# Kernel optimization log

Measured on AMD Instinct MI355X. Metric: run time of the kernel, lower is better.

The kernel has to match this reference:

```python
import jax, jax.numpy as jnp
import numpy as np

HEAD_DIM = 64
N_HEADS = 16
DIM = 1024
EPS = 1e-6
GRID = 32  # make_axial_pos(32, 32)


def _make_theta(head_dim=HEAD_DIM, n_heads=N_HEADS):
    hd8 = head_dim // 8
    nh2 = n_heads // 2
    freqs = np.exp(np.linspace(np.log(np.pi), np.log(10 * np.pi), hd8 * nh2 + 1)[:-1])
    freqs = freqs.reshape(hd8, nh2).T  # (nh2, hd8)
    # axial positions on a 32x32 grid, cell centers in [-1, 1]
    p = np.linspace(-1.0, 1.0, GRID + 1)
    p = (p[:-1] + p[1:]) / 2
    pos = np.stack(np.meshgrid(p, p, indexing='ij'), axis=-1).reshape(GRID * GRID, 2)
    pos = np.concatenate([np.zeros((1, 2)), pos], axis=0)  # (1025, 2)
    th1 = np.concatenate([pos[:-1, None, 0:1] * freqs, pos[:-1, None, 1:2] * freqs], axis=-1)
    th2 = np.concatenate([pos[1:, None, 0:1] * freqs, pos[1:, None, 1:2] * freqs], axis=-1)
    # (seq=1024, n_heads, head_dim//4)
    return np.concatenate([th1, th2], axis=1).astype(np.float32)


def setup_inputs() -> dict:
    key = jax.random.key(0)
    k1, k2, k3 = jax.random.split(key, 3)
    B, S = 8, 1024
    x = jax.random.normal(k1, (B, S, DIM), dtype=jnp.float32)
    scale = jnp.ones((DIM,), dtype=jnp.float32)
    w_qkv = jax.random.normal(k2, (3 * DIM, DIM), dtype=jnp.float32) * 0.02
    w_out = jax.random.normal(k3, (DIM, DIM), dtype=jnp.float32) * 0.02
    theta = jnp.asarray(_make_theta())
    return {"x": x, "scale": scale, "w_qkv": w_qkv, "w_out": w_out, "theta": theta}


def _rms_norm(x, scale, eps):
    xf = x.astype(jnp.float32)
    mean_sq = jnp.mean(xf * xf, axis=-1, keepdims=True)
    s = scale.astype(jnp.float32) * jax.lax.rsqrt(mean_sq + eps)
    return x * s.astype(x.dtype)


def _rope(x, theta):
    # x: (B, H, S, D); theta: (H, S, d) with d = D // 4 -> rotates first D//2 dims
    d = theta.shape[-1]
    cos = jnp.cos(theta)
    sin = jnp.sin(theta)
    x1, x2, rest = x[..., :d], x[..., d:2 * d], x[..., 2 * d:]
    y1 = x1 * cos - x2 * sin
    y2 = x2 * cos + x1 * sin
    return jnp.concatenate([y1, y2, rest], axis=-1)


def reference(x, scale, w_qkv, w_out, theta):
    B, S, dim = x.shape
    H = N_HEADS
    D = dim // H
    skip = x
    xn = _rms_norm(x, scale, EPS)
    qkv = xn @ w_qkv.T                                  # (B, S, 3*dim)
    qkv = qkv.reshape(B, S, 3, H, D).transpose(0, 3, 2, 1, 4)  # (B, H, 3, S, D)
    q, k, v = qkv[:, :, 0], qkv[:, :, 1], qkv[:, :, 2]  # (B, H, S, D)
    th = theta[:S].transpose(1, 0, 2)                   # (H, S, D//4)
    q = _rope(q, th)
    k = _rope(k, th)
    scores = jnp.einsum('bhsd,bhtd->bhst', q, k) / jnp.sqrt(jnp.float32(D))
    causal = jnp.tril(jnp.ones((S, S), dtype=bool))
    scores = jnp.where(causal, scores, jnp.finfo(scores.dtype).min)
    attn = jax.nn.softmax(scores, axis=-1)
    o = jnp.einsum('bhst,bhtd->bhsd', attn, v)          # (B, H, S, D)
    o = o.transpose(0, 2, 1, 3).reshape(B, S, dim)
    return o @ w_out.T + skip
```

## Files before the change

kernel.cpp:

```cpp
#include <hip/hip_runtime.h>
#include <hip/hip_bf16.h>
#include <cstdint>

typedef short short8 __attribute__((ext_vector_type(8)));
typedef float f32x4 __attribute__((ext_vector_type(4)));
typedef unsigned uint4v __attribute__((ext_vector_type(4)));

#define MFMA16(a, b, c) __builtin_amdgcn_mfma_f32_16x16x32_bf16((a), (b), (c), 0, 0, 0)

__device__ __forceinline__ unsigned short f2b(float f) {
    __hip_bfloat16 h = __float2bfloat16(f);
    return __builtin_bit_cast(unsigned short, h);
}

__device__ __forceinline__ void gl_lds16(const void* g, void* l) {
    __builtin_amdgcn_global_load_lds((const __attribute__((address_space(1))) void*)g,
                                     (__attribute__((address_space(3))) void*)l, 16, 0, 0);
}

#define QSC 0.18033688011112042f

__global__ void rmsnorm_kernel(const float* __restrict__ x, const float* __restrict__ scale,
                               unsigned short* __restrict__ xn) {
    const int row = blockIdx.x;
    const int tid = threadIdx.x;
    const float4* xr = (const float4*)(x + (size_t)row * 1024);
    float4 vx = xr[tid];
    float ss = vx.x * vx.x + vx.y * vx.y + vx.z * vx.z + vx.w * vx.w;
#pragma unroll
    for (int m = 1; m < 64; m <<= 1) ss += __shfl_xor(ss, m);
    __shared__ float wsum[4];
    if ((tid & 63) == 0) wsum[tid >> 6] = ss;
    __syncthreads();
    float tot = wsum[0] + wsum[1] + wsum[2] + wsum[3];
    float rs = rsqrtf(tot * (1.0f / 1024.0f) + 1e-6f);
    const float4* sr = (const float4*)scale;
    float4 sv = sr[tid];
    ushort4 r;
    r.x = f2b(vx.x * sv.x * rs);
    r.y = f2b(vx.y * sv.y * rs);
    r.z = f2b(vx.z * sv.z * rs);
    r.w = f2b(vx.w * sv.w * rs);
    *(ushort4*)(xn + (size_t)row * 1024 + tid * 4) = r;
}

__global__ void f2b_kernel(const float* __restrict__ in, unsigned short* __restrict__ outp, int n4) {
    int i = blockIdx.x * 256 + threadIdx.x;
    if (i < n4) {
        float4 vv = ((const float4*)in)[i];
        ushort4 r;
        r.x = f2b(vv.x);
        r.y = f2b(vv.y);
        r.z = f2b(vv.z);
        r.w = f2b(vv.w);
        ((ushort4*)outp)[i] = r;
    }
}

constexpr int BM = 128, BN = 128, BK = 64, KDIM = 1024, NT = KDIM / BK;

template <int EPI>
__launch_bounds__(256, 4) __global__
    void gemm_bt(const unsigned short* __restrict__ A, const unsigned short* __restrict__ Bw,
                 unsigned short* __restrict__ qo, unsigned short* __restrict__ ko,
                 unsigned short* __restrict__ vo, const float* __restrict__ skip,
                 float* __restrict__ out, const float* __restrict__ theta) {
    __shared__ unsigned short As[BM * BK];
    __shared__ unsigned short Bs[BN * BK];
    const int tid = threadIdx.x;
    const int lane = tid & 63, w = tid >> 6;
    const int wr = w >> 1, wc = w & 1;
    const int lr = lane & 15, lg = lane >> 4;
    constexpr int NBX = (EPI == 0) ? 24 : 8;
    const int f = blockIdx.x;
    const int xcd = f & 7, wloc = f >> 3;
    const int g = xcd * (NBX * 8) + wloc;
    const int bx = g % NBX, by = g / NBX;
    const int m0 = by * BM;
    const int n0 = bx * BN;
    const int NCOL = (EPI == 0) ? 3072 : 1024;

    f32x4 acc[4][4] = {};

    auto stage = [&](int kt) {
        const int k0 = kt * BK;
#pragma unroll
        for (int i = 0; i < 4; ++i) {
            int seg = i * 256 + tid;
            int row = seg >> 3, c8 = (seg & 7) ^ (row & 7);
            gl_lds16(A + (size_t)(m0 + row) * KDIM + k0 + c8 * 8, &As[(i * 256 + w * 64) * 8]);
            gl_lds16(Bw + (size_t)(n0 + row) * KDIM + k0 + c8 * 8, &Bs[(i * 256 + w * 64) * 8]);
        }
    };

    for (int kt = 0; kt < NT; ++kt) {
        stage(kt);
        __syncthreads();
#pragma unroll
        for (int kkc = 0; kkc < 2; ++kkc) {
            short8 a[4], b[4];
            const int slot = ((kkc * 4 + lg) ^ (lr & 7)) * 8;
#pragma unroll
            for (int m = 0; m < 4; ++m)
                a[m] = *(const short8*)&As[(wr * 64 + m * 16 + lr) * BK + slot];
#pragma unroll
            for (int n = 0; n < 4; ++n)
                b[n] = *(const short8*)&Bs[(wc * 64 + n * 16 + lr) * BK + slot];
#pragma unroll
            for (int m = 0; m < 4; ++m)
#pragma unroll
                for (int n = 0; n < 4; ++n) acc[m][n] = MFMA16(a[m], b[n], acc[m][n]);
        }
        __syncthreads();
    }

    if (EPI == 0) {
        const int colb = n0 + wc * 64;
        const int c = colb >> 10, h = (colb >> 6) & 15;
#pragma unroll
        for (int m = 0; m < 4; ++m) {
            int grow0 = m0 + wr * 64 + m * 16 + lg * 4;
            int b = grow0 >> 10, s0 = grow0 & 1023;
            if (c == 2) {
#pragma unroll
                for (int n = 0; n < 4; ++n) {
                    int d = n * 16 + lr;
                    ushort4 r;
                    r.x = f2b(acc[m][n][0]);
                    r.y = f2b(acc[m][n][1]);
                    r.z = f2b(acc[m][n][2]);
                    r.w = f2b(acc[m][n][3]);
                    *(ushort4*)&vo[(((size_t)(b * 16 + h)) * 64 + d) * 1024 + s0] = r;
                }
            } else {
                unsigned short* dst = (c == 0) ? qo : ko;
                float sc = (c == 0) ? QSC : 1.0f;
#pragma unroll
                for (int j = 0; j < 4; ++j) {
                    int s = s0 + j;
                    float th = theta[((s * 16 + h) << 4) + lr];
                    float sn, cs;
                    __sincosf(th, &sn, &cs);
                    float x1 = acc[m][0][j], x2 = acc[m][1][j];
                    size_t rowb = (((size_t)(b * 16 + h)) * 1024 + s) * 64;
                    dst[rowb + lr]      = f2b((x1 * cs - x2 * sn) * sc);
                    dst[rowb + 16 + lr] = f2b((x2 * cs + x1 * sn) * sc);
                    dst[rowb + 32 + lr] = f2b(acc[m][2][j] * sc);
                    dst[rowb + 48 + lr] = f2b(acc[m][3][j] * sc);
                }
            }
        }
    } else {
#pragma unroll
        for (int m = 0; m < 4; ++m)
#pragma unroll
            for (int n = 0; n < 4; ++n) {
                int gcol = n0 + wc * 64 + n * 16 + lr;
#pragma unroll
                for (int j = 0; j < 4; ++j) {
                    int grow = m0 + wr * 64 + m * 16 + lg * 4 + j;
                    size_t idx = (size_t)grow * NCOL + gcol;
                    out[idx] = acc[m][n][j] + skip[idx];
                }
            }
    }
}

__launch_bounds__(512, 4) __global__
    void attn_kernel(const unsigned short* __restrict__ q, const unsigned short* __restrict__ k,
                     const unsigned short* __restrict__ vt, unsigned short* __restrict__ o) {
    constexpr int S = 1024, D = 64;
    __shared__ unsigned short Ks[2][64 * 64];
    __shared__ unsigned short Vs[2][64 * 64];
    __shared__ float Lls[8][32];
    const int tid = threadIdx.x, lane = tid & 63, w = tid >> 6;
    const int lr = lane & 15, lg = lane >> 4;
    const int f = blockIdx.x;
    constexpr int qmap4[4] = {3, 2, 0, 1};
    const int qb = qmap4[f >> 7];
    const int bh = (f & 7) * 16 + ((f >> 3) & 15);
    const int qs = qb * 256;
    const size_t base = (size_t)bh * (S * D);
    const int wrow0 = qs + w * 32;

    short8 qf[2][2];
#pragma unroll
    for (int m = 0; m < 2; ++m) {
        const unsigned short* qp = q + base + (size_t)(wrow0 + m * 16 + lr) * D;
        qf[m][0] = *(const short8*)(qp + lg * 8);
        qf[m][1] = *(const short8*)(qp + 32 + lg * 8);
    }

    f32x4 of[2][4] = {};
    float mrun[2] = {-1e30f, -1e30f};
    float lrun[2] = {0.f, 0.f};

    const int nkt = 4 * qb + 4;

    const int srow = tid >> 3, sc8 = (tid & 7) ^ (srow & 7);
    auto stageK = [&](int buf, int kt) {
        gl_lds16(k + base + (size_t)(kt * 64 + srow) * D + sc8 * 8, &Ks[buf][w * 512]);
    };
    auto stageV = [&](int buf, int kt) {
        gl_lds16(vt + base + (size_t)srow * S + kt * 64 + sc8 * 8, &Vs[buf][w * 512]);
    };

    stageK(0, 0);
    stageV(0, 0);
    __syncthreads();

    for (int kt = 0; kt < nkt; ++kt) {
        const int b = kt & 1;
        if (kt + 1 < nkt) {
            stageK(b ^ 1, kt + 1);
            stageV(b ^ 1, kt + 1);
        }

        if (kt * 64 <= wrow0 + 31) {
            f32x4 sf[2][4] = {};
            __builtin_amdgcn_s_setprio(1);
#pragma unroll
            for (int n = 0; n < 4; ++n) {
                const int r = n * 16 + lr;
#pragma unroll
                for (int kkc = 0; kkc < 2; ++kkc) {
                    short8 kf = *(const short8*)&Ks[b][r * 64 + (((kkc * 4 + lg) ^ (lr & 7)) * 8)];
#pragma unroll
                    for (int m = 0; m < 2; ++m) sf[m][n] = MFMA16(kf, qf[m][kkc], sf[m][n]);
                }
            }
            __builtin_amdgcn_s_setprio(0);

            if (kt * 64 + 63 > wrow0) {
#pragma unroll
                for (int m = 0; m < 2; ++m)
#pragma unroll
                    for (int n = 0; n < 4; ++n)
#pragma unroll
                        for (int j = 0; j < 4; ++j) {
                            int t = kt * 64 + 16 * n + lg * 4 + j;
                            int qr = wrow0 + m * 16 + lr;
                            if (t > qr) sf[m][n][j] = -1e30f;
                        }
            }

#pragma unroll
            for (int m = 0; m < 2; ++m) {
                float mx = -1e30f;
#pragma unroll
                for (int n = 0; n < 4; ++n)
                    mx = fmaxf(mx, fmaxf(fmaxf(sf[m][n][0], sf[m][n][1]),
                                         fmaxf(sf[m][n][2], sf[m][n][3])));
                mx = fmaxf(mx, __shfl_xor(mx, 16));
                mx = fmaxf(mx, __shfl_xor(mx, 32));

                if (__any(mx > mrun[m] + 8.0f)) {
                    float newm = fmaxf(mrun[m], mx);
                    float sc = __builtin_amdgcn_exp2f(mrun[m] - newm);
                    mrun[m] = newm;
                    float psum = 0.f;
#pragma unroll
                    for (int n = 0; n < 4; ++n)
#pragma unroll
                        for (int j = 0; j < 4; ++j) {
                            float p = __builtin_amdgcn_exp2f(sf[m][n][j] - newm);
                            sf[m][n][j] = p;
                            psum += p;
                        }
                    lrun[m] = lrun[m] * sc + psum;
#pragma unroll
                    for (int n2 = 0; n2 < 4; ++n2) of[m][n2] *= sc;
                } else {
                    float mo = mrun[m];
                    float psum = 0.f;
#pragma unroll
                    for (int n = 0; n < 4; ++n)
#pragma unroll
                        for (int j = 0; j < 4; ++j) {
                            float p = __builtin_amdgcn_exp2f(sf[m][n][j] - mo);
                            sf[m][n][j] = p;
                            psum += p;
                        }
                    lrun[m] += psum;
                }
            }

            short8 pa[2][2];
#pragma unroll
            for (int m = 0; m < 2; ++m) {
                unsigned Dk[4][2];
#pragma unroll
                for (int n = 0; n < 4; ++n)
#pragma unroll
                    for (int w2 = 0; w2 < 2; ++w2)
                        Dk[n][w2] = (unsigned)f2b(sf[m][n][2 * w2]) |
                                    ((unsigned)f2b(sf[m][n][2 * w2 + 1]) << 16);
#pragma unroll
                for (int n1 = 0; n1 < 2; ++n1) {
                    unsigned fr[4];
#pragma unroll
                    for (int w2 = 0; w2 < 2; ++w2) {
                        unsigned X0 = Dk[2 * n1][w2];
                        unsigned X1 = Dk[2 * n1 + 1][w2];
                        asm("v_permlane32_swap_b32 %0, %1" : "+v"(X0), "+v"(X1));
                        asm("v_permlane16_swap_b32 %0, %1" : "+v"(X0), "+v"(X1));
                        fr[w2] = X0;
                        fr[2 + w2] = X1;
                    }
                    uint4v t4 = {fr[0], fr[1], fr[2], fr[3]};
                    pa[m][n1] = __builtin_bit_cast(short8, t4);
                }
            }

            __builtin_amdgcn_s_setprio(1);
#pragma unroll
            for (int kkc = 0; kkc < 2; ++kkc) {
#pragma unroll
                for (int n2 = 0; n2 < 4; ++n2) {
                    const int r = n2 * 16 + lr;
                    short8 bv = *(const short8*)&Vs[b][r * 64 + (((kkc * 4 + lg) ^ (lr & 7)) * 8)];
#pragma unroll
                    for (int m = 0; m < 2; ++m) of[m][n2] = MFMA16(pa[m][kkc], bv, of[m][n2]);
                }
            }
            __builtin_amdgcn_s_setprio(0);
        }

        __syncthreads();
    }

#pragma unroll
    for (int m = 0; m < 2; ++m) {
        float l = lrun[m];
        l += __shfl_xor(l, 16);
        l += __shfl_xor(l, 32);
        Lls[w][m * 16 + lr] = l;
    }
    const int bb = bh >> 4, h = bh & 15;
#pragma unroll
    for (int m = 0; m < 2; ++m)
#pragma unroll
        for (int j = 0; j < 4; ++j) {
            float inv = 1.f / Lls[w][m * 16 + lg * 4 + j];
            int orow = wrow0 + m * 16 + lg * 4 + j;
            size_t ob = ((size_t)(bb * 1024 + orow)) * 1024 + h * 64;
#pragma unroll
            for (int n2 = 0; n2 < 4; ++n2)
                o[ob + n2 * 16 + lr] = f2b(of[m][n2][j] * inv);
        }
}

extern "C" void kernel_launch(void* const* d_in, const int* in_sizes, int n_in, void* d_out,
                              int out_size, void* d_ws, size_t ws_size, hipStream_t stream) {
    const float* x = (const float*)d_in[0];
    const float* scale = (const float*)d_in[1];
    const float* w_qkv = (const float*)d_in[2];
    const float* w_out = (const float*)d_in[3];
    const float* theta = (const float*)d_in[4];
    float* out = (float*)d_out;

    char* p = (char*)d_ws;
    unsigned short* xn = (unsigned short*)p;      p += (size_t)8192 * 1024 * 2;
    unsigned short* wqb = (unsigned short*)p;     p += (size_t)3072 * 1024 * 2;
    unsigned short* wob = (unsigned short*)p;     p += (size_t)1024 * 1024 * 2;
    unsigned short* qb_ = (unsigned short*)p;     p += (size_t)128 * 1024 * 64 * 2;
    unsigned short* kb_ = (unsigned short*)p;     p += (size_t)128 * 1024 * 64 * 2;
    unsigned short* vb_ = (unsigned short*)p;     p += (size_t)128 * 1024 * 64 * 2;
    unsigned short* ob_ = (unsigned short*)p;     p += (size_t)8192 * 1024 * 2;

    rmsnorm_kernel<<<8192, 256, 0, stream>>>(x, scale, xn);
    f2b_kernel<<<3072, 256, 0, stream>>>(w_qkv, wqb, 786432);
    f2b_kernel<<<1024, 256, 0, stream>>>(w_out, wob, 262144);
    gemm_bt<0><<<1536, 256, 0, stream>>>(xn, wqb, qb_, kb_, vb_, nullptr, nullptr, theta);
    attn_kernel<<<512, 512, 0, stream>>>(qb_, kb_, vb_, ob_);
    gemm_bt<1><<<512, 256, 0, stream>>>(ob_, wob, nullptr, nullptr, nullptr, x, out, nullptr);
}
```

Baseline: 151.8 us.

## Replace QKV GEMM with 256x256-tile 8-wave kernel and phased double buffering

```diff
diff --git a/kernel.cpp b/kernel.cpp
--- a/kernel.cpp
+++ b/kernel.cpp
@@ -166,6 +166,168 @@
     }
 }
 
+__launch_bounds__(512, 2) __global__
+    void gemm256_qkv(const unsigned short* __restrict__ A, const unsigned short* __restrict__ Bw,
+                     unsigned short* __restrict__ qo, unsigned short* __restrict__ ko,
+                     unsigned short* __restrict__ vo, const float* __restrict__ theta) {
+    __shared__ unsigned short As[2][256 * 64];
+    __shared__ unsigned short Bs[2][256 * 64];
+    const int tid = threadIdx.x;
+    const int lane = tid & 63, w = tid >> 6;
+    const int wm = w >> 2, wn = w & 3;
+    const int lr = lane & 15, lg = lane >> 4;
+    const int f = blockIdx.x;
+    const int xcd = f & 7, wloc = f >> 3;
+    const int g = xcd * 48 + wloc;
+    const int bx = g % 12, by = g / 12;
+    const int m0 = by * 256, n0 = bx * 256;
+
+    f32x4 acc[2][2][4][2] = {};
+
+#define STAGE_A(buf, kt, h)                                                            \
+    {                                                                                  \
+        _Pragma("unroll") for (int i = 0; i < 2; ++i) {                                \
+            int seg = i * 512 + tid;                                                   \
+            int row = seg >> 3, cs = (seg & 7) ^ (row & 7);                            \
+            gl_lds16(A + (size_t)(m0 + (h)*128 + row) * 1024 + (kt)*64 + cs * 8,       \
+                     &As[buf][(h)*8192 + (i * 512 + w * 64) * 8]);                     \
+        }                                                                              \
+    }
+#define STAGE_B(buf, kt, h)                                                            \
+    {                                                                                  \
+        _Pragma("unroll") for (int i = 0; i < 2; ++i) {                                \
+            int seg = i * 512 + tid;                                                   \
+            int row = seg >> 3, cs = (seg & 7) ^ (row & 7);                            \
+            gl_lds16(Bw + (size_t)(n0 + (h)*128 + row) * 1024 + (kt)*64 + cs * 8,      \
+                     &Bs[buf][(h)*8192 + (i * 512 + w * 64) * 8]);                     \
+        }                                                                              \
+    }
+#define VMW(N) asm volatile("s_waitcnt vmcnt(" #N ")" ::: "memory")
+#define BARX()                              \
+    {                                       \
+        asm volatile("" ::: "memory");      \
+        __builtin_amdgcn_s_barrier();       \
+        asm volatile("" ::: "memory");      \
+    }
+#define QUAD(buf, mh, nh)                                                              \
+    {                                                                                  \
+        short8 afr[4][2], bfr[2][2];                                                   \
+        _Pragma("unroll") for (int m = 0; m < 4; ++m) _Pragma("unroll") for (int kk =  \
+                                                                               0;      \
+                                                                           kk < 2;    \
+                                                                           ++kk) {    \
+            int r = (mh)*128 + wm * 64 + m * 16 + lr;                                  \
+            int slot = (kk * 4 + lg) ^ (r & 7);                                        \
+            afr[m][kk] = *(const short8*)&As[buf][r * 64 + slot * 8];                  \
+        }                                                                              \
+        _Pragma("unroll") for (int n = 0; n < 2; ++n) _Pragma("unroll") for (int kk =  \
+                                                                               0;      \
+                                                                           kk < 2;    \
+                                                                           ++kk) {    \
+            int c = (nh)*128 + wn * 32 + n * 16 + lr;                                  \
+            int slot = (kk * 4 + lg) ^ (c & 7);                                        \
+            bfr[n][kk] = *(const short8*)&Bs[buf][c * 64 + slot * 8];                  \
+        }                                                                              \
+        __builtin_amdgcn_s_setprio(1);                                                 \
+        _Pragma("unroll") for (int kk = 0; kk < 2; ++kk)                               \
+            _Pragma("unroll") for (int m = 0; m < 4; ++m)                              \
+                _Pragma("unroll") for (int n = 0; n < 2; ++n)                          \
+                    acc[mh][nh][m][n] = MFMA16(afr[m][kk], bfr[n][kk],                 \
+                                               acc[mh][nh][m][n]);                     \
+        __builtin_amdgcn_s_setprio(0);                                                 \
+    }
+#define PHASE(S, VMN, buf, mh, nh) \
+    {                              \
+        S;                         \
+        VMW(VMN);                  \
+        BARX();                    \
+        QUAD(buf, mh, nh);         \
+        BARX();                    \
+    }
+
+    STAGE_A(0, 0, 0);
+    STAGE_B(0, 0, 0);
+    STAGE_A(0, 0, 1);
+    STAGE_B(0, 0, 1);
+
+    for (int i = 0; i < 7; ++i) {
+        const int tb = 2 * i + 1, tc = 2 * i + 2;
+        PHASE(STAGE_A(1, tb, 0), 6, 0, 0, 0);
+        PHASE(STAGE_B(1, tb, 0), 6, 0, 1, 0);
+        PHASE(STAGE_A(1, tb, 1), 6, 0, 0, 1);
+        PHASE(STAGE_B(1, tb, 1), 6, 0, 1, 1);
+        PHASE(STAGE_A(0, tc, 0), 6, 1, 0, 0);
+        PHASE(STAGE_B(0, tc, 0), 6, 1, 1, 0);
+        PHASE(STAGE_A(0, tc, 1), 6, 1, 0, 1);
+        PHASE(STAGE_B(0, tc, 1), 6, 1, 1, 1);
+    }
+    PHASE(STAGE_A(1, 15, 0), 6, 0, 0, 0);
+    PHASE(STAGE_B(1, 15, 0), 6, 0, 1, 0);
+    PHASE(STAGE_A(1, 15, 1), 6, 0, 0, 1);
+    PHASE(STAGE_B(1, 15, 1), 6, 0, 1, 1);
+    PHASE(((void)0), 4, 1, 0, 0);
+    PHASE(((void)0), 2, 1, 1, 0);
+    PHASE(((void)0), 0, 1, 0, 1);
+    PHASE(((void)0), 0, 1, 1, 1);
+
+#undef PHASE
+#undef QUAD
+#undef BARX
+#undef VMW
+#undef STAGE_B
+#undef STAGE_A
+
+#pragma unroll
+    for (int nh = 0; nh < 2; ++nh) {
+        const int X = n0 + nh * 128 + wn * 32;
+        const int c = X >> 10, hh = (X >> 6) & 15;
+        const bool lowh = (X & 63) == 0;
+#pragma unroll
+        for (int mh = 0; mh < 2; ++mh)
+#pragma unroll
+            for (int m = 0; m < 4; ++m) {
+                int grow0 = m0 + mh * 128 + wm * 64 + m * 16 + lg * 4;
+                int bb = grow0 >> 10, s0 = grow0 & 1023;
+                if (c == 2) {
+#pragma unroll
+                    for (int n = 0; n < 2; ++n) {
+                        int d = (X & 63) + n * 16 + lr;
+                        ushort4 r4;
+                        r4.x = f2b(acc[mh][nh][m][n][0]);
+                        r4.y = f2b(acc[mh][nh][m][n][1]);
+                        r4.z = f2b(acc[mh][nh][m][n][2]);
+                        r4.w = f2b(acc[mh][nh][m][n][3]);
+                        *(ushort4*)&vo[(((size_t)(bb * 16 + hh)) * 64 + d) * 1024 + s0] = r4;
+                    }
+                } else {
+                    unsigned short* dst = (c == 0) ? qo : ko;
+                    float sc = (c == 0) ? QSC : 1.0f;
+                    if (lowh) {
+#pragma unroll
+                        for (int j = 0; j < 4; ++j) {
+                            int s = s0 + j;
+                            float th = theta[((s * 16 + hh) << 4) + lr];
+                            float sn, cs2;
+                            __sincosf(th, &sn, &cs2);
+                            float x1 = acc[mh][nh][m][0][j], x2 = acc[mh][nh][m][1][j];
+                            size_t rowb = (((size_t)(bb * 16 + hh)) * 1024 + s) * 64;
+                            dst[rowb + lr]      = f2b((x1 * cs2 - x2 * sn) * sc);
+                            dst[rowb + 16 + lr] = f2b((x2 * cs2 + x1 * sn) * sc);
+                        }
+                    } else {
+#pragma unroll
+                        for (int j = 0; j < 4; ++j) {
+                            int s = s0 + j;
+                            size_t rowb = (((size_t)(bb * 16 + hh)) * 1024 + s) * 64;
+                            dst[rowb + 32 + lr] = f2b(acc[mh][nh][m][0][j] * sc);
+                            dst[rowb + 48 + lr] = f2b(acc[mh][nh][m][1][j] * sc);
+                        }
+                    }
+                }
+            }
+    }
+}
+
 __launch_bounds__(512, 4) __global__
     void attn_kernel(const unsigned short* __restrict__ q, const unsigned short* __restrict__ k,
                      const unsigned short* __restrict__ vt, unsigned short* __restrict__ o) {
@@ -371,7 +533,7 @@
     rmsnorm_kernel<<<8192, 256, 0, stream>>>(x, scale, xn);
     f2b_kernel<<<3072, 256, 0, stream>>>(w_qkv, wqb, 786432);
     f2b_kernel<<<1024, 256, 0, stream>>>(w_out, wob, 262144);
-    gemm_bt<0><<<1536, 256, 0, stream>>>(xn, wqb, qb_, kb_, vb_, nullptr, nullptr, theta);
+    gemm256_qkv<<<384, 512, 0, stream>>>(xn, wqb, qb_, kb_, vb_, theta);
     attn_kernel<<<512, 512, 0, stream>>>(qb_, kb_, vb_, ob_);
     gemm_bt<1><<<512, 256, 0, stream>>>(ob_, wob, nullptr, nullptr, nullptr, x, out, nullptr);
 }
```

New measurement: 182.6 us. +20.3%, slower.
